# Kernel optimization log

Measured on AMD Instinct MI355X. Metric: run time of the kernel, lower is better.

## Reference

```python
import jax, jax.numpy as jnp
import numpy as np

LOGIT_SCALE = 1.0
REDUCTION = "mean"

N, H, V = 4096, 512, 50257


def setup_inputs() -> dict:
    key = jax.random.key(0)
    k1, k2, k3, k4 = jax.random.split(key, 4)
    x = jax.random.normal(k1, (N, H), dtype=jnp.float32)
    targets = jax.random.normal(k2, (N, V), dtype=jnp.float32)
    weight = jax.random.normal(k3, (V, H), dtype=jnp.float32) * 0.02
    bias = jax.random.normal(k4, (V,), dtype=jnp.float32) * 0.02
    return {"x": x, "targets": targets, "weight": weight, "bias": bias}


def reference(x, targets, weight, bias):
    # logits = x @ W^T + b  -> [N, V]
    logits = jnp.einsum("nh,vh->nv", x, weight) + bias
    scaled = logits * LOGIT_SCALE
    # logsumexp over vocab for both predicted and target logits (fp32)
    lse_logits = jax.nn.logsumexp(scaled, axis=-1)                      # [N]
    lse_targets = jax.nn.logsumexp(targets, axis=-1)                    # [N]
    # original: .nan_to_num(nan=inf) -> rows with nan targets contribute 0
    lse_targets = jnp.where(jnp.isnan(lse_targets), jnp.inf, lse_targets)
    p_target = jnp.exp(targets - lse_targets[:, None])                  # softmax(targets)
    log_p_pred = scaled - lse_logits[:, None]                           # log_softmax(scaled logits)
    per_row_loss = -jnp.sum(p_target * log_p_pred, axis=-1)             # [N]
    loss = per_row_loss.sum()
    if REDUCTION == "mean":
        loss = loss / N
    return loss
```

## Files before the change

kernel.cpp:

```cpp
#include <hip/hip_runtime.h>
#include <hip/hip_bf16.h>

#define N_ROWS 4096
#define H_DIM  512
#define V_DIM  50257
#define BM 128
#define BN 128
#define BK 64
#define NSTEP (H_DIM / BK)
#define VT_TOTAL 393
#define V_PAD (VT_TOTAL * BN)
#define NCHUNK 131
#define LOG2E 1.4426950408889634f
#define BUF0 0
#define BUF1 32768
#define LBASE 32768

#define VMCNT4() asm volatile("s_waitcnt vmcnt(4)" ::: "memory")
#define VMCNT0() asm volatile("s_waitcnt vmcnt(0)" ::: "memory")
#define LGKM0()  asm volatile("s_waitcnt lgkmcnt(0)" ::: "memory")
#define BARRIER() __builtin_amdgcn_s_barrier()

typedef __attribute__((ext_vector_type(8))) short short8;
typedef __attribute__((ext_vector_type(4))) float f32x4;

static __device__ __forceinline__ unsigned short f2bf(float f) {
  unsigned u = __float_as_uint(f);
  u = (u + 0x7fffu + ((u >> 16) & 1u)) >> 16;
  return (unsigned short)u;
}

static __device__ __forceinline__ void gload_lds16(const void* g, void* l) {
  __builtin_amdgcn_global_load_lds(
      (const __attribute__((address_space(1))) void*)g,
      (__attribute__((address_space(3))) void*)l, 16, 0, 0);
}

__global__ void convert_kernel(const float* __restrict__ X,
                               const float* __restrict__ W,
                               __hip_bfloat16* __restrict__ Xb,
                               __hip_bfloat16* __restrict__ Wb) {
  const long wtot8 = (long)V_PAD * H_DIM / 8;
  const long xtot8 = (long)N_ROWS * H_DIM / 8;
  long i = (long)blockIdx.x * blockDim.x + threadIdx.x;
  unsigned short o[8];
  if (i < wtot8) {
    long base = i * 8;
    long row = base >> 9;
    if (row < V_DIM) {
      const float4* s = (const float4*)(W + base);
      float4 a = s[0], b = s[1];
      o[0]=f2bf(a.x); o[1]=f2bf(a.y); o[2]=f2bf(a.z); o[3]=f2bf(a.w);
      o[4]=f2bf(b.x); o[5]=f2bf(b.y); o[6]=f2bf(b.z); o[7]=f2bf(b.w);
    } else {
      #pragma unroll
      for (int k = 0; k < 8; ++k) o[k] = 0;
    }
    *(short8*)(Wb + base) = *(const short8*)o;
  } else if (i < wtot8 + xtot8) {
    long base = (i - wtot8) * 8;
    const float4* s = (const float4*)(X + base);
    float4 a = s[0], b = s[1];
    o[0]=f2bf(a.x); o[1]=f2bf(a.y); o[2]=f2bf(a.z); o[3]=f2bf(a.w);
    o[4]=f2bf(b.x); o[5]=f2bf(b.y); o[6]=f2bf(b.z); o[7]=f2bf(b.w);
    *(short8*)(Xb + base) = *(const short8*)o;
  }
}

template <bool GUARD>
static __device__ __forceinline__ void chunk_stats(
    const float (&Lraw)[16], const f32x4 (&T)[4], int gcol0,
    float& mlr, float& slr, float& mtr, float& str, float& ddr) {
  float Lv[16], Tv[16];
  #pragma unroll
  for (int k = 0; k < 16; ++k) {
    const bool ok = !GUARD || (gcol0 + k < V_DIM);
    Lv[k] = ok ? Lraw[k] : -1e30f;
    Tv[k] = ok ? T[k >> 2][k & 3] : -1e30f;
  }
  float g = Lv[0];
  #pragma unroll
  for (int k = 1; k < 16; ++k) g = fmaxf(g, Lv[k]);
  if (g > mlr + 12.f) { slr *= exp2f((mlr - g) * LOG2E); mlr = g; }
  float bl = mlr * LOG2E;
  float ss = 0.f;
  #pragma unroll
  for (int k = 0; k < 16; ++k) ss += exp2f(__builtin_fmaf(Lv[k], LOG2E, -bl));
  slr += ss;
  float gt = Tv[0];
  #pragma unroll
  for (int k = 1; k < 16; ++k) gt = fmaxf(gt, Tv[k]);
  if (gt > mtr + 12.f) {
    float sc = exp2f((mtr - gt) * LOG2E);
    str *= sc; ddr *= sc; mtr = gt;
  }
  float bt = mtr * LOG2E;
  float s2 = 0.f, d2 = 0.f;
  #pragma unroll
  for (int k = 0; k < 16; ++k) {
    float e = exp2f(__builtin_fmaf(Tv[k], LOG2E, -bt));
    s2 += e;
    d2 = __builtin_fmaf(e, Lv[k], d2);
  }
  str += s2; ddr += d2;
}

template <bool GUARD>
static __device__ __forceinline__ void stream_tile(
    const float* __restrict__ targets, const char* __restrict__ Lrow,
    long growVD, int vbase, int q32, int rsw, long tlim,
    float& mlr, float& slr, float& mtr, float& str, float& ddr) {
  f32x4 T0[4], T1[4];
  #pragma unroll
  for (int c = 0; c < 4; ++c) {
    long off = growVD + vbase + q32 + c * 4;
    if (GUARD) off = off > tlim ? tlim : off;
    T0[c] = *(const f32x4*)(targets + off);
  }
  #pragma unroll
  for (int c = 0; c < 4; ++c) {
    long off = growVD + vbase + q32 + 16 + c * 4;
    if (GUARD) off = off > tlim ? tlim : off;
    T1[c] = *(const f32x4*)(targets + off);
  }
  #pragma unroll
  for (int i = 0; i < 2; ++i) {
    const int ob = (q32 << 1) + (i << 5);
    short8 l0 = *(const short8*)(Lrow + ((ob) ^ rsw));
    short8 l1 = *(const short8*)(Lrow + ((ob + 16) ^ rsw));
    float Lraw[16];
    #pragma unroll
    for (int e = 0; e < 8; ++e) {
      Lraw[e]     = __uint_as_float(((unsigned)(unsigned short)l0[e]) << 16);
      Lraw[e + 8] = __uint_as_float(((unsigned)(unsigned short)l1[e]) << 16);
    }
    if (i == 0)
      chunk_stats<GUARD>(Lraw, T0, vbase + q32,      mlr, slr, mtr, str, ddr);
    else
      chunk_stats<GUARD>(Lraw, T1, vbase + q32 + 16, mlr, slr, mtr, str, ddr);
  }
}

__global__ __launch_bounds__(512, 4)
void fused_kernel(const __hip_bfloat16* __restrict__ Xb,
                  const __hip_bfloat16* __restrict__ Wb,
                  const float* __restrict__ bias,
                  const float* __restrict__ targets,
                  float* __restrict__ partials) {
  __shared__ __align__(16) char smem[65536];

  const int tid  = threadIdx.x;
  const int lane = tid & 63;
  const int wid  = tid >> 6;
  const int wm   = wid >> 2;
  const int wn   = wid & 3;
  const int q    = lane >> 4;
  const int c15  = lane & 15;
  const int brow = blockIdx.x;
  const int chunk = blockIdx.y;

  float mlr = -1e30f, slr = 0.f, mtr = -1e30f, str = 0.f, ddr = 0.f;

  const int srow8 = tid >> 3;
  const int soff  = ((tid & 7) ^ (srow8 & 7)) * 8;
  const __hip_bfloat16* asrc = Xb + (long)(brow * BM + srow8) * H_DIM + soff;

  const int rm      = (c15 & 7) << 4;
  const int arow_b  = (wm * 64 + c15) * 128;
  const int brow_b  = (wn * 32 + c15) * 128;

  auto stage = [&](int bufb, const __hip_bfloat16* a_s,
                   const __hip_bfloat16* b_s, int kk) {
    #pragma unroll
    for (int i = 0; i < 2; ++i)
      gload_lds16(a_s + (long)i * 64 * H_DIM + kk,
                  smem + bufb + i * 8192 + tid * 16);
    #pragma unroll
    for (int i = 0; i < 2; ++i)
      gload_lds16(b_s + (long)i * 64 * H_DIM + kk,
                  smem + bufb + 16384 + i * 8192 + tid * 16);
  };

  const int srow  = tid >> 2;
  const int quart = tid & 3;
  const int q32   = quart * 32;
  const long grow   = (long)(brow * BM + srow);
  const long growVD = grow * V_DIM;
  const long tlim   = (long)N_ROWS * V_DIM - 4;
  const char* Lrow  = smem + LBASE + srow * 256;
  const int rsw     = (srow & 7) << 4;

  const __hip_bfloat16* bsrc = Wb + (long)(chunk * BN + srow8) * H_DIM + soff;
  stage(BUF0, asrc, bsrc, 0);

  #pragma unroll 1
  for (int vt = chunk; vt < VT_TOTAL; vt += NCHUNK) {
    const int vbase = vt * BN;
    const int v0 = vbase + wn * 32 + q * 4;
    const bool last = (vt + NCHUNK >= VT_TOTAL);
    const __hip_bfloat16* bsrc_next =
        Wb + (long)((vt + NCHUNK) * BN + srow8) * H_DIM + soff;

    f32x4 acc[4][2];
    #pragma unroll
    for (int a = 0; a < 4; ++a)
      #pragma unroll
      for (int b = 0; b < 2; ++b)
        acc[a][b] = (f32x4){0.f, 0.f, 0.f, 0.f};

    #pragma unroll
    for (int ks = 0; ks < NSTEP; ++ks) {
      const int cb = (ks & 1) ? BUF1 : BUF0;
      const int nb = cb ^ 32768;
      if (ks < NSTEP - 1)
        stage(nb, asrc, bsrc, (ks + 1) * BK);
      else if (!last)
        stage(nb, asrc, bsrc_next, 0);

      if (ks == NSTEP - 1 && last) { VMCNT0(); } else { VMCNT4(); }
      BARRIER();

      #pragma unroll
      for (int s = 0; s < 2; ++s) {
        short8 xf[4], wf[2];
        #pragma unroll
        for (int a = 0; a < 4; ++a)
          xf[a] = *(const short8*)(smem + cb + arow_b + a * 2048 +
                                   ((s * 64 + q * 16) ^ rm));
        #pragma unroll
        for (int b = 0; b < 2; ++b)
          wf[b] = *(const short8*)(smem + cb + 16384 + brow_b + b * 2048 +
                                   ((s * 64 + q * 16) ^ rm));
        #pragma unroll
        for (int a = 0; a < 4; ++a)
          #pragma unroll
          for (int b = 0; b < 2; ++b)
            acc[a][b] = __builtin_amdgcn_mfma_f32_16x16x32_bf16(
                wf[b], xf[a], acc[a][b], 0, 0, 0);
      }
      LGKM0();
      BARRIER();
    }
    bsrc = bsrc_next;

    f32x4 bp[2];
    #pragma unroll
    for (int b = 0; b < 2; ++b) {
      int bo = v0 + b * 16;
      bo = bo > (V_DIM - 4) ? (V_DIM - 4) : bo;
      bp[b] = *(const f32x4*)(bias + bo);
    }
    #pragma unroll
    for (int a = 0; a < 4; ++a) {
      const int row = wm * 64 + a * 16 + c15;
      char* rb = smem + LBASE + row * 256;
      #pragma unroll
      for (int b = 0; b < 2; ++b) {
        uint2 w;
        w.x = (unsigned)f2bf(acc[a][b][0] + bp[b][0]) |
              ((unsigned)f2bf(acc[a][b][1] + bp[b][1]) << 16);
        w.y = (unsigned)f2bf(acc[a][b][2] + bp[b][2]) |
              ((unsigned)f2bf(acc[a][b][3] + bp[b][3]) << 16);
        const int o = wn * 64 + b * 32 + q * 8;
        *(uint2*)(rb + (o ^ rm)) = w;
      }
    }
    LGKM0();
    BARRIER();

    if (vt == VT_TOTAL - 1)
      stream_tile<true >(targets, Lrow, growVD, vbase, q32, rsw, tlim,
                         mlr, slr, mtr, str, ddr);
    else
      stream_tile<false>(targets, Lrow, growVD, vbase, q32, rsw, tlim,
                         mlr, slr, mtr, str, ddr);
    LGKM0();
    BARRIER();
  }

  #pragma unroll
  for (int off = 1; off <= 2; off <<= 1) {
    float ml2 = __shfl_xor(mlr, off);
    float sl2 = __shfl_xor(slr, off);
    float mt2 = __shfl_xor(mtr, off);
    float st2 = __shfl_xor(str, off);
    float dd2 = __shfl_xor(ddr, off);
    float nm = fmaxf(mlr, ml2);
    slr = slr * exp2f((mlr - nm) * LOG2E) + sl2 * exp2f((ml2 - nm) * LOG2E);
    mlr = nm;
    float nmt = fmaxf(mtr, mt2);
    float e1 = exp2f((mtr - nmt) * LOG2E);
    float e2 = exp2f((mt2 - nmt) * LOG2E);
    str = str * e1 + st2 * e2;
    ddr = ddr * e1 + dd2 * e2;
    mtr = nmt;
  }
  if (quart == 0) {
    float* o = partials + (grow * NCHUNK + chunk) * 5;
    o[0] = mlr; o[1] = slr; o[2] = mtr; o[3] = str; o[4] = ddr;
  }
}

__global__ void rowloss_kernel(const float* __restrict__ partials,
                               float* __restrict__ rowloss) {
  int r = blockIdx.x * blockDim.x + threadIdx.x;
  if (r >= N_ROWS) return;
  const float* p = partials + (long)r * NCHUNK * 5;
  float ml = -1e30f, sl = 0.f, mt = -1e30f, st = 0.f, dd = 0.f;
  for (int c = 0; c < NCHUNK; ++c) {
    float ml2 = p[0], sl2 = p[1], mt2 = p[2], st2 = p[3], dd2 = p[4];
    p += 5;
    float nm = fmaxf(ml, ml2);
    sl = sl * exp2f((ml - nm) * LOG2E) + sl2 * exp2f((ml2 - nm) * LOG2E);
    ml = nm;
    float nmt = fmaxf(mt, mt2);
    float e1 = exp2f((mt - nmt) * LOG2E);
    float e2 = exp2f((mt2 - nmt) * LOG2E);
    st = st * e1 + st2 * e2;
    dd = dd * e1 + dd2 * e2;
    mt = nmt;
  }
  float lse = ml + logf(sl);
  rowloss[r] = lse - dd / st;
}

__global__ void final_kernel(const float* __restrict__ rowloss,
                             float* __restrict__ out) {
  __shared__ float sm[4];
  float s = 0.f;
  for (int i = threadIdx.x; i < N_ROWS; i += 256) s += rowloss[i];
  #pragma unroll
  for (int off = 32; off > 0; off >>= 1) s += __shfl_down(s, off);
  if ((threadIdx.x & 63) == 0) sm[threadIdx.x >> 6] = s;
  __syncthreads();
  if (threadIdx.x == 0) out[0] = (sm[0] + sm[1] + sm[2] + sm[3]) * (1.0f / (float)N_ROWS);
}

extern "C" void kernel_launch(void* const* d_in, const int* in_sizes, int n_in,
                              void* d_out, int out_size, void* d_ws, size_t ws_size,
                              hipStream_t stream) {
  const float* x       = (const float*)d_in[0];
  const float* targets = (const float*)d_in[1];
  const float* weight  = (const float*)d_in[2];
  const float* bias    = (const float*)d_in[3];
  float* out = (float*)d_out;

  char* ws = (char*)d_ws;
  __hip_bfloat16* Wb = (__hip_bfloat16*)ws;
  size_t off = (size_t)V_PAD * H_DIM * 2;
  __hip_bfloat16* Xb = (__hip_bfloat16*)(ws + off);
  off += (size_t)N_ROWS * H_DIM * 2;
  float* partials = (float*)(ws + off);
  off += (size_t)N_ROWS * NCHUNK * 5 * sizeof(float);
  float* rowloss = (float*)(ws + off);

  convert_kernel<<<13600, 256, 0, stream>>>(x, weight, Xb, Wb);
  dim3 grid(N_ROWS / BM, NCHUNK);
  fused_kernel<<<grid, 512, 0, stream>>>(Xb, Wb, bias, targets, partials);
  rowloss_kernel<<<N_ROWS / 256, 256, 0, stream>>>(partials, rowloss);
  final_kernel<<<1, 256, 0, stream>>>(rowloss, out);
}
```

Before: 537.3 us.

## Overlap target streaming and softmax stats with next tile's GEMM k-loop

Moves the logits tile into its own LDS region, growing dynamic shared memory to 96 KB, so the previous tile's target loads and online softmax statistics can run inside the next tile's MFMA k-loop. Target loads are software-pipelined with double buffering and custom vmcnt waits. The 3-tile loop is fully unrolled with bias prefetched up front. Occupancy bound drops from 4 to 2 blocks per CU, trading fewer waves for hiding the memory-bound target stream behind compute.

```diff
diff --git a/kernel.cpp b/kernel.cpp
--- a/kernel.cpp
+++ b/kernel.cpp
@@ -7,22 +7,27 @@
 #define BM 128
 #define BN 128
 #define BK 64
-#define NSTEP (H_DIM / BK)
+#define NSTEP 8
 #define VT_TOTAL 393
 #define V_PAD (VT_TOTAL * BN)
 #define NCHUNK 131
 #define LOG2E 1.4426950408889634f
-#define BUF0 0
-#define BUF1 32768
-#define LBASE 32768
-
-#define VMCNT4() asm volatile("s_waitcnt vmcnt(4)" ::: "memory")
-#define VMCNT0() asm volatile("s_waitcnt vmcnt(0)" ::: "memory")
+#define LBASE 65536
+#define SMEM_BYTES 98304
+
 #define LGKM0()  asm volatile("s_waitcnt lgkmcnt(0)" ::: "memory")
 #define BARRIER() __builtin_amdgcn_s_barrier()
 
 typedef __attribute__((ext_vector_type(8))) short short8;
 typedef __attribute__((ext_vector_type(4))) float f32x4;
+
+template <int N>
+static __device__ __forceinline__ void vmw() {
+  if constexpr (N == 0)      asm volatile("s_waitcnt vmcnt(0)" ::: "memory");
+  else if constexpr (N == 1) asm volatile("s_waitcnt vmcnt(1)" ::: "memory");
+  else if constexpr (N == 4) asm volatile("s_waitcnt vmcnt(4)" ::: "memory");
+  else                       asm volatile("s_waitcnt vmcnt(5)" ::: "memory");
+}
 
 static __device__ __forceinline__ unsigned short f2bf(float f) {
   unsigned u = __float_as_uint(f);
@@ -67,87 +72,47 @@
   }
 }
 
-template <bool GUARD>
-static __device__ __forceinline__ void chunk_stats(
-    const float (&Lraw)[16], const f32x4 (&T)[4], int gcol0,
-    float& mlr, float& slr, float& mtr, float& str, float& ddr) {
-  float Lv[16], Tv[16];
-  #pragma unroll
-  for (int k = 0; k < 16; ++k) {
-    const bool ok = !GUARD || (gcol0 + k < V_DIM);
-    Lv[k] = ok ? Lraw[k] : -1e30f;
-    Tv[k] = ok ? T[k >> 2][k & 3] : -1e30f;
-  }
-  float g = Lv[0];
-  #pragma unroll
-  for (int k = 1; k < 16; ++k) g = fmaxf(g, Lv[k]);
-  if (g > mlr + 12.f) { slr *= exp2f((mlr - g) * LOG2E); mlr = g; }
-  float bl = mlr * LOG2E;
-  float ss = 0.f;
-  #pragma unroll
-  for (int k = 0; k < 16; ++k) ss += exp2f(__builtin_fmaf(Lv[k], LOG2E, -bl));
-  slr += ss;
-  float gt = Tv[0];
-  #pragma unroll
-  for (int k = 1; k < 16; ++k) gt = fmaxf(gt, Tv[k]);
-  if (gt > mtr + 12.f) {
-    float sc = exp2f((mtr - gt) * LOG2E);
-    str *= sc; ddr *= sc; mtr = gt;
-  }
-  float bt = mtr * LOG2E;
-  float s2 = 0.f, d2 = 0.f;
-  #pragma unroll
-  for (int k = 0; k < 16; ++k) {
-    float e = exp2f(__builtin_fmaf(Tv[k], LOG2E, -bt));
-    s2 += e;
-    d2 = __builtin_fmaf(e, Lv[k], d2);
-  }
-  str += s2; ddr += d2;
-}
-
-template <bool GUARD>
-static __device__ __forceinline__ void stream_tile(
-    const float* __restrict__ targets, const char* __restrict__ Lrow,
-    long growVD, int vbase, int q32, int rsw, long tlim,
-    float& mlr, float& slr, float& mtr, float& str, float& ddr) {
-  f32x4 T0[4], T1[4];
-  #pragma unroll
-  for (int c = 0; c < 4; ++c) {
-    long off = growVD + vbase + q32 + c * 4;
-    if (GUARD) off = off > tlim ? tlim : off;
-    T0[c] = *(const f32x4*)(targets + off);
-  }
-  #pragma unroll
-  for (int c = 0; c < 4; ++c) {
-    long off = growVD + vbase + q32 + 16 + c * 4;
-    if (GUARD) off = off > tlim ? tlim : off;
-    T1[c] = *(const f32x4*)(targets + off);
-  }
-  #pragma unroll
-  for (int i = 0; i < 2; ++i) {
-    const int ob = (q32 << 1) + (i << 5);
-    short8 l0 = *(const short8*)(Lrow + ((ob) ^ rsw));
-    short8 l1 = *(const short8*)(Lrow + ((ob + 16) ^ rsw));
-    float Lraw[16];
-    #pragma unroll
-    for (int e = 0; e < 8; ++e) {
-      Lraw[e]     = __uint_as_float(((unsigned)(unsigned short)l0[e]) << 16);
-      Lraw[e + 8] = __uint_as_float(((unsigned)(unsigned short)l1[e]) << 16);
-    }
-    if (i == 0)
-      chunk_stats<GUARD>(Lraw, T0, vbase + q32,      mlr, slr, mtr, str, ddr);
-    else
-      chunk_stats<GUARD>(Lraw, T1, vbase + q32 + 16, mlr, slr, mtr, str, ddr);
-  }
-}
-
-__global__ __launch_bounds__(512, 4)
+static __device__ __forceinline__ void stats4(
+    const f32x4& T, uint2 lw, int gcol0,
+    float& ml, float& sl, float& mt, float& st, float& dd) {
+  float Lv[4], Tv[4];
+  unsigned lu[2] = {lw.x, lw.y};
+  #pragma unroll
+  for (int j = 0; j < 4; ++j) {
+    unsigned h = (lu[j >> 1] >> ((j & 1) * 16)) & 0xffffu;
+    float lvf = __uint_as_float(h << 16);
+    bool ok = (gcol0 + j < V_DIM);
+    Lv[j] = ok ? lvf : -1e30f;
+    Tv[j] = ok ? T[j] : -1e30f;
+  }
+  float g = fmaxf(fmaxf(Lv[0], Lv[1]), fmaxf(Lv[2], Lv[3]));
+  if (g > ml + 12.f) { sl *= exp2f((ml - g) * LOG2E); ml = g; }
+  float bl = ml * LOG2E;
+  sl += exp2f(__builtin_fmaf(Lv[0], LOG2E, -bl))
+      + exp2f(__builtin_fmaf(Lv[1], LOG2E, -bl))
+      + exp2f(__builtin_fmaf(Lv[2], LOG2E, -bl))
+      + exp2f(__builtin_fmaf(Lv[3], LOG2E, -bl));
+  float gt = fmaxf(fmaxf(Tv[0], Tv[1]), fmaxf(Tv[2], Tv[3]));
+  if (gt > mt + 12.f) {
+    float sc = exp2f((mt - gt) * LOG2E);
+    st *= sc; dd *= sc; mt = gt;
+  }
+  float bt = mt * LOG2E;
+  #pragma unroll
+  for (int j = 0; j < 4; ++j) {
+    float e = exp2f(__builtin_fmaf(Tv[j], LOG2E, -bt));
+    st += e;
+    dd = __builtin_fmaf(e, Lv[j], dd);
+  }
+}
+
+__global__ __launch_bounds__(512, 2)
 void fused_kernel(const __hip_bfloat16* __restrict__ Xb,
                   const __hip_bfloat16* __restrict__ Wb,
                   const float* __restrict__ bias,
                   const float* __restrict__ targets,
                   float* __restrict__ partials) {
-  __shared__ __align__(16) char smem[65536];
+  extern __shared__ __align__(16) char smem[];
 
   const int tid  = threadIdx.x;
   const int lane = tid & 63;
@@ -159,47 +124,63 @@
   const int brow = blockIdx.x;
   const int chunk = blockIdx.y;
 
-  float mlr = -1e30f, slr = 0.f, mtr = -1e30f, str = 0.f, ddr = 0.f;
+  float ml = -1e30f, sl = 0.f, mt = -1e30f, st = 0.f, dd = 0.f;
 
   const int srow8 = tid >> 3;
   const int soff  = ((tid & 7) ^ (srow8 & 7)) * 8;
   const __hip_bfloat16* asrc = Xb + (long)(brow * BM + srow8) * H_DIM + soff;
-
-  const int rm      = (c15 & 7) << 4;
-  const int arow_b  = (wm * 64 + c15) * 128;
-  const int brow_b  = (wn * 32 + c15) * 128;
-
-  auto stage = [&](int bufb, const __hip_bfloat16* a_s,
-                   const __hip_bfloat16* b_s, int kk) {
+  const __hip_bfloat16* wb0  = Wb + (long)((long)chunk * BN + srow8) * H_DIM + soff;
+  const long WSTRIDE = (long)NCHUNK * BN * H_DIM;
+
+  const int rm     = (c15 & 7) << 4;
+  const int arow_b = (wm * 64 + c15) * 128;
+  const int brow_b = (wn * 32 + c15) * 128;
+
+  auto stage = [&](int bufb, const __hip_bfloat16* wsrcp, int kk) {
     #pragma unroll
     for (int i = 0; i < 2; ++i)
-      gload_lds16(a_s + (long)i * 64 * H_DIM + kk,
+      gload_lds16(asrc + (long)i * 64 * H_DIM + kk,
                   smem + bufb + i * 8192 + tid * 16);
     #pragma unroll
     for (int i = 0; i < 2; ++i)
-      gload_lds16(b_s + (long)i * 64 * H_DIM + kk,
+      gload_lds16(wsrcp + (long)i * 64 * H_DIM + kk,
                   smem + bufb + 16384 + i * 8192 + tid * 16);
   };
 
-  const int srow  = tid >> 2;
+  const int strow = tid >> 2;
   const int quart = tid & 3;
-  const int q32   = quart * 32;
-  const long grow   = (long)(brow * BM + srow);
+  const int scol  = quart * 32;
+  const long grow   = (long)(brow * BM + strow);
   const long growVD = grow * V_DIM;
   const long tlim   = (long)N_ROWS * V_DIM - 4;
-  const char* Lrow  = smem + LBASE + srow * 256;
-  const int rsw     = (srow & 7) << 4;
-
-  const __hip_bfloat16* bsrc = Wb + (long)(chunk * BN + srow8) * H_DIM + soff;
-  stage(BUF0, asrc, bsrc, 0);
-
-  #pragma unroll 1
-  for (int vt = chunk; vt < VT_TOTAL; vt += NCHUNK) {
-    const int vbase = vt * BN;
-    const int v0 = vbase + wn * 32 + q * 4;
-    const bool last = (vt + NCHUNK >= VT_TOTAL);
-    const __hip_bfloat16* bsrc_next =
-        Wb + (long)((vt + NCHUNK) * BN + srow8) * H_DIM + soff;
+  const char* Lrow  = smem + LBASE + strow * 256;
+  const int rsw     = (strow & 7) << 4;
+
+  f32x4 bp[3][2];
+  #pragma unroll
+  for (int g = 0; g < 3; ++g) {
+    const int v0g = (chunk + g * NCHUNK) * BN + wn * 32 + q * 4;
+    #pragma unroll
+    for (int b = 0; b < 2; ++b) {
+      int bo = v0g + b * 16;
+      bo = bo > (V_DIM - 4) ? (V_DIM - 4) : bo;
+      bp[g][b] = *(const f32x4*)(bias + bo);
+    }
+  }
+
+  f32x4 tbuf[2];
+  auto loadT = [&](f32x4& dst, int g, int c) {
+    long off = growVD + (long)(chunk + g * NCHUNK) * BN + scol + c * 4;
+    off = off > tlim ? tlim : off;
+    dst = *(const f32x4*)(targets + off);
+  };
+
+  stage(0, wb0, 0);
+
+  #pragma unroll
+  for (int g = 0; g < 3; ++g) {
+    const __hip_bfloat16* wcur = wb0 + (long)g * WSTRIDE;
+    const int gcPrev = (chunk + (g - 1) * NCHUNK) * BN + scol;
 
     f32x4 acc[4][2];
     #pragma unroll
@@ -210,14 +191,18 @@
 
     #pragma unroll
     for (int ks = 0; ks < NSTEP; ++ks) {
-      const int cb = (ks & 1) ? BUF1 : BUF0;
+      const int cb = (ks & 1) ? 32768 : 0;
       const int nb = cb ^ 32768;
       if (ks < NSTEP - 1)
-        stage(nb, asrc, bsrc, (ks + 1) * BK);
-      else if (!last)
-        stage(nb, asrc, bsrc_next, 0);
-
-      if (ks == NSTEP - 1 && last) { VMCNT0(); } else { VMCNT4(); }
+        stage(nb, wcur, (ks + 1) * BK);
+      else if (g < 2)
+        stage(nb, wcur + WSTRIDE, 0);
+      if (g > 0 && ks < NSTEP - 1) loadT(tbuf[(ks + 1) & 1], g - 1, ks + 1);
+      if (ks == NSTEP - 1)         loadT(tbuf[0], g, 0);
+
+      if (ks == NSTEP - 1 && g == 2)      vmw<1>();
+      else if (g == 0 && ks < NSTEP - 1)  vmw<4>();
+      else                                vmw<5>();
       BARRIER();
 
       #pragma unroll
@@ -238,18 +223,15 @@
             acc[a][b] = __builtin_amdgcn_mfma_f32_16x16x32_bf16(
                 wf[b], xf[a], acc[a][b], 0, 0, 0);
       }
+
+      if (g > 0) {
+        uint2 lw = *(const uint2*)(Lrow + ((scol * 2 + ks * 8) ^ rsw));
+        stats4(tbuf[ks & 1], lw, gcPrev + ks * 4, ml, sl, mt, st, dd);
+      }
       LGKM0();
       BARRIER();
     }
-    bsrc = bsrc_next;
-
-    f32x4 bp[2];
-    #pragma unroll
-    for (int b = 0; b < 2; ++b) {
-      int bo = v0 + b * 16;
-      bo = bo > (V_DIM - 4) ? (V_DIM - 4) : bo;
-      bp[b] = *(const f32x4*)(bias + bo);
-    }
+
     #pragma unroll
     for (int a = 0; a < 4; ++a) {
       const int row = wm * 64 + a * 16 + c15;
@@ -257,47 +239,44 @@
       #pragma unroll
       for (int b = 0; b < 2; ++b) {
         uint2 w;
-        w.x = (unsigned)f2bf(acc[a][b][0] + bp[b][0]) |
-              ((unsigned)f2bf(acc[a][b][1] + bp[b][1]) << 16);
-        w.y = (unsigned)f2bf(acc[a][b][2] + bp[b][2]) |
-              ((unsigned)f2bf(acc[a][b][3] + bp[b][3]) << 16);
+        w.x = (unsigned)f2bf(acc[a][b][0] + bp[g][b][0]) |
+              ((unsigned)f2bf(acc[a][b][1] + bp[g][b][1]) << 16);
+        w.y = (unsigned)f2bf(acc[a][b][2] + bp[g][b][2]) |
+              ((unsigned)f2bf(acc[a][b][3] + bp[g][b][3]) << 16);
         const int o = wn * 64 + b * 32 + q * 8;
         *(uint2*)(rb + (o ^ rm)) = w;
       }
     }
     LGKM0();
     BARRIER();
-
-    if (vt == VT_TOTAL - 1)
-      stream_tile<true >(targets, Lrow, growVD, vbase, q32, rsw, tlim,
-                         mlr, slr, mtr, str, ddr);
-    else
-      stream_tile<false>(targets, Lrow, growVD, vbase, q32, rsw, tlim,
-                         mlr, slr, mtr, str, ddr);
-    LGKM0();
-    BARRIER();
+  }
+
+  const int gcT2 = (chunk + 2 * NCHUNK) * BN + scol;
+  #pragma unroll
+  for (int c = 0; c < 8; ++c) {
+    if (c < 7) loadT(tbuf[(c + 1) & 1], 2, c + 1);
+    if (c < 7) vmw<1>(); else vmw<0>();
+    uint2 lw = *(const uint2*)(Lrow + ((scol * 2 + c * 8) ^ rsw));
+    stats4(tbuf[c & 1], lw, gcT2 + c * 4, ml, sl, mt, st, dd);
   }
 
   #pragma unroll
   for (int off = 1; off <= 2; off <<= 1) {
-    float ml2 = __shfl_xor(mlr, off);
-    float sl2 = __shfl_xor(slr, off);
-    float mt2 = __shfl_xor(mtr, off);
-    float st2 = __shfl_xor(str, off);
-    float dd2 = __shfl_xor(ddr, off);
-    float nm = fmaxf(mlr, ml2);
-    slr = slr * exp2f((mlr - nm) * LOG2E) + sl2 * exp2f((ml2 - nm) * LOG2E);
-    mlr = nm;
-    float nmt = fmaxf(mtr, mt2);
-    float e1 = exp2f((mtr - nmt) * LOG2E);
-    float e2 = exp2f((mt2 - nmt) * LOG2E);
-    str = str * e1 + st2 * e2;
-    ddr = ddr * e1 + dd2 * e2;
-    mtr = nmt;
+    float ml2 = __shfl_xor(ml, off), sl2 = __shfl_xor(sl, off);
+    float mt2 = __shfl_xor(mt, off), st2 = __shfl_xor(st, off);
+    float dd2 = __shfl_xor(dd, off);
+    float nm = fmaxf(ml, ml2);
+    sl = sl * exp2f((ml - nm) * LOG2E) + sl2 * exp2f((ml2 - nm) * LOG2E);
+    ml = nm;
+    float nmt = fmaxf(mt, mt2);
+    float e1 = exp2f((mt - nmt) * LOG2E), e2 = exp2f((mt2 - nmt) * LOG2E);
+    st = st * e1 + st2 * e2;
+    dd = dd * e1 + dd2 * e2;
+    mt = nmt;
   }
   if (quart == 0) {
     float* o = partials + (grow * NCHUNK + chunk) * 5;
-    o[0] = mlr; o[1] = slr; o[2] = mtr; o[3] = str; o[4] = ddr;
+    o[0] = ml; o[1] = sl; o[2] = mt; o[3] = st; o[4] = dd;
   }
 }
 
@@ -354,9 +333,13 @@
   off += (size_t)N_ROWS * NCHUNK * 5 * sizeof(float);
   float* rowloss = (float*)(ws + off);
 
+  (void)hipFuncSetAttribute((const void*)fused_kernel,
+                            hipFuncAttributeMaxDynamicSharedMemorySize,
+                            SMEM_BYTES);
+
   convert_kernel<<<13600, 256, 0, stream>>>(x, weight, Xb, Wb);
   dim3 grid(N_ROWS / BM, NCHUNK);
-  fused_kernel<<<grid, 512, 0, stream>>>(Xb, Wb, bias, targets, partials);
+  fused_kernel<<<grid, 512, SMEM_BYTES, stream>>>(Xb, Wb, bias, targets, partials);
   rowloss_kernel<<<N_ROWS / 256, 256, 0, stream>>>(partials, rowloss);
   final_kernel<<<1, 256, 0, stream>>>(rowloss, out);
 }
```

New measurement: 797.8 us. 1.48x slower.
